# Performance work log

Hardware: AMD Instinct MI355X
Metric: run time of the kernel (lower is better)

## Reference

```python
import jax, jax.numpy as jnp
import numpy as np

B, S, D = 2, 2048, 1024
E, H = 1024, 16
HD = E // H  # head_dim = 64


def setup_inputs() -> dict:
    key = jax.random.key(0)
    k1, k2, k3 = jax.random.split(key, 3)
    x = jax.random.normal(k1, (B, S, D), dtype=jnp.float32)
    # torch Linear weights: [out_features, in_features], xavier_uniform init, zero bias
    lim_qkv = float(np.sqrt(6.0 / (D + 3 * E)))
    w_qkv = jax.random.uniform(k2, (3 * E, D), minval=-lim_qkv, maxval=lim_qkv, dtype=jnp.float32)
    b_qkv = jnp.zeros((3 * E,), dtype=jnp.float32)
    lim_o = float(np.sqrt(6.0 / (E + D)))
    w_out = jax.random.uniform(k3, (D, E), minval=-lim_o, maxval=lim_o, dtype=jnp.float32)
    b_out = jnp.zeros((D,), dtype=jnp.float32)
    return {"x": x, "w_qkv": w_qkv, "b_qkv": b_qkv, "w_out": w_out, "b_out": b_out}


def reference(x, w_qkv, b_qkv, w_out, b_out):
    b, s, _ = x.shape
    qkv = x @ w_qkv.T + b_qkv                       # [B,S,3E]
    qkv = qkv.reshape(b, s, H, 3 * HD).transpose(0, 2, 1, 3)  # [B,H,S,3*HD]
    q, k, v = jnp.split(qkv, 3, axis=-1)            # each [B,H,S,HD]
    # NOTE: source divides by head_dim, not sqrt(head_dim)
    logits = jnp.einsum('bhqd,bhkd->bhqk', q, k) / HD
    attn = jax.nn.softmax(logits, axis=-1)          # [B,H,S,S]
    vals = jnp.einsum('bhqk,bhkd->bhqd', attn, v)   # [B,H,S,HD]
    vals = vals.transpose(0, 2, 1, 3).reshape(b, s, E)
    out = vals @ w_out.T + b_out                    # [B,S,D]
    return out, attn
```

## Files before the change

kernel.cpp:

```cpp
#include <hip/hip_runtime.h>


typedef unsigned short u16;
typedef __attribute__((ext_vector_type(8))) short bf16x8;
typedef __attribute__((ext_vector_type(4))) float f32x4;
typedef __attribute__((ext_vector_type(4))) unsigned int u32x4;
typedef __attribute__((ext_vector_type(4))) unsigned short u16x4;

__device__ __forceinline__ u16 f2b(float f) {
  unsigned u = __builtin_bit_cast(unsigned, f);
  unsigned r = u + 0x7FFFu + ((u >> 16) & 1u);
  return (u16)(r >> 16);
}

__global__ __launch_bounds__(256) void cast_bf16(const float* __restrict__ in,
                                                 u16* __restrict__ out, int n4) {
  int i = blockIdx.x * 256 + threadIdx.x;
  if (i >= n4) return;
  f32x4 v = ((const f32x4*)in)[i];
  u16x4 o;
  o.x = f2b(v.x); o.y = f2b(v.y); o.z = f2b(v.z); o.w = f2b(v.w);
  ((u16x4*)out)[i] = o;
}

template <int EPI>
__global__ __launch_bounds__(256) void gemm_nt(
    const u16* __restrict__ A, const u16* __restrict__ B,
    const float* __restrict__ bias, float* __restrict__ Cout,
    u16* __restrict__ outq, u16* __restrict__ outk, u16* __restrict__ outvT,
    int M, int N, int K) {
  __shared__ u16 lA[128][40];
  __shared__ u16 lB[128][40];
  const int t = threadIdx.x;
  const int lane = t & 63;
  const int w = t >> 6;
  const int wr = w >> 1, wc = w & 1;
  const int l15 = lane & 15, lg = lane >> 4;
  const int m0 = blockIdx.y * 128;
  const int n0 = blockIdx.x * 128;
  const int ldrow = t >> 1;
  const int ldel = (t & 1) * 16;

  f32x4 acc[4][4] = {};

  for (int k0 = 0; k0 < K; k0 += 32) {
    const u16* ga = A + (size_t)(m0 + ldrow) * K + k0 + ldel;
    const u16* gb = B + (size_t)(n0 + ldrow) * K + k0 + ldel;
    u32x4 va0 = *(const u32x4*)ga;
    u32x4 va1 = *(const u32x4*)(ga + 8);
    u32x4 vb0 = *(const u32x4*)gb;
    u32x4 vb1 = *(const u32x4*)(gb + 8);
    *(u32x4*)&lA[ldrow][ldel]     = va0;
    *(u32x4*)&lA[ldrow][ldel + 8] = va1;
    *(u32x4*)&lB[ldrow][ldel]     = vb0;
    *(u32x4*)&lB[ldrow][ldel + 8] = vb1;
    __syncthreads();
    bf16x8 af[4], bf[4];
#pragma unroll
    for (int i = 0; i < 4; i++)
      af[i] = *(const bf16x8*)&lA[64 * wr + 16 * i + l15][8 * lg];
#pragma unroll
    for (int j = 0; j < 4; j++)
      bf[j] = *(const bf16x8*)&lB[64 * wc + 16 * j + l15][8 * lg];
#pragma unroll
    for (int i = 0; i < 4; i++)
#pragma unroll
      for (int j = 0; j < 4; j++)
        acc[i][j] = __builtin_amdgcn_mfma_f32_16x16x32_bf16(af[i], bf[j], acc[i][j], 0, 0, 0);
    __syncthreads();
  }

  const int r0 = lg * 4;
#pragma unroll
  for (int i = 0; i < 4; i++) {
    const int m = m0 + 64 * wr + 16 * i + r0;
#pragma unroll
    for (int j = 0; j < 4; j++) {
      const int n = n0 + 64 * wc + 16 * j + l15;
      const float bv = bias[n];
      if (EPI == 0) {
#pragma unroll
        for (int r = 0; r < 4; r++)
          Cout[(size_t)(m + r) * N + n] = acc[i][j][r] + bv;
      } else {
        const int h = n / 192;
        const int rem = n - h * 192;
        const int which = rem >> 6;
        const int d = rem & 63;
        const int b = m >> 11;
        const int s = m & 2047;
        const size_t bh = (size_t)b * 16 + h;
        u16 o[4];
#pragma unroll
        for (int r = 0; r < 4; r++) o[r] = f2b(acc[i][j][r] + bv);
        if (which == 0) {
#pragma unroll
          for (int r = 0; r < 4; r++)
            outq[(bh * 2048 + s + r) * 64 + d] = o[r];
        } else if (which == 1) {
#pragma unroll
          for (int r = 0; r < 4; r++)
            outk[(bh * 2048 + s + r) * 64 + d] = o[r];
        } else {
          u16x4 pk; pk.x = o[0]; pk.y = o[1]; pk.z = o[2]; pk.w = o[3];
          *(u16x4*)&outvT[(bh * 64 + d) * 2048 + s] = pk;
        }
      }
    }
  }
}

__global__ __launch_bounds__(256) void attn_fused(
    const u16* __restrict__ q, const u16* __restrict__ kk, const u16* __restrict__ vT,
    float* __restrict__ attn, u16* __restrict__ valsb) {
  constexpr int S = 2048, HD = 64;
  __shared__ u16 lQ[64][72];
  __shared__ u16 lK[128][72];
  __shared__ u16 lV[64][136];
  __shared__ u16 lP[64][136];

  const int t = threadIdx.x;
  const int lane = t & 63;
  const int w = t >> 6;
  const int l15 = lane & 15, lg = lane >> 4;
  const int qb = blockIdx.x;
  const int bh = blockIdx.y;
  const size_t qkbase = (size_t)bh * S * HD;
  const float scale = 1.0f / 64.0f;

  {
#pragma unroll
    for (int p = 0; p < 2; p++) {
      int cc = t + p * 256;
      int row = cc >> 3, ch = cc & 7;
      *(u32x4*)&lQ[row][ch * 8] =
          *(const u32x4*)&q[qkbase + (size_t)(qb * 64 + row) * HD + ch * 8];
    }
  }
  __syncthreads();
  bf16x8 aq[2];
#pragma unroll
  for (int s2 = 0; s2 < 2; s2++)
    aq[s2] = *(const bf16x8*)&lQ[16 * w + l15][32 * s2 + 8 * lg];

  float rs[4] = {0.f, 0.f, 0.f, 0.f};

  for (int kt = 0; kt < 16; ++kt) {
    __syncthreads();
#pragma unroll
    for (int p = 0; p < 4; p++) {
      int cc = t + p * 256;
      int row = cc >> 3, ch = cc & 7;
      *(u32x4*)&lK[row][ch * 8] =
          *(const u32x4*)&kk[qkbase + (size_t)(kt * 128 + row) * HD + ch * 8];
    }
    __syncthreads();
#pragma unroll
    for (int j = 0; j < 8; j++) {
      f32x4 sa = {0.f, 0.f, 0.f, 0.f};
#pragma unroll
      for (int s2 = 0; s2 < 2; s2++) {
        bf16x8 bk = *(const bf16x8*)&lK[16 * j + l15][32 * s2 + 8 * lg];
        sa = __builtin_amdgcn_mfma_f32_16x16x32_bf16(aq[s2], bk, sa, 0, 0, 0);
      }
#pragma unroll
      for (int r = 0; r < 4; r++) rs[r] += __expf(sa[r] * scale);
    }
  }
#pragma unroll
  for (int dlt = 1; dlt < 16; dlt <<= 1)
#pragma unroll
    for (int r = 0; r < 4; r++) rs[r] += __shfl_xor(rs[r], dlt, 64);
  float inv[4];
#pragma unroll
  for (int r = 0; r < 4; r++) inv[r] = 1.0f / rs[r];

  f32x4 vacc[4] = {};
  const size_t vbase = (size_t)bh * HD * S;
  for (int kt = 0; kt < 16; ++kt) {
    __syncthreads();
#pragma unroll
    for (int p = 0; p < 4; p++) {
      int cc = t + p * 256;
      int row = cc >> 3, ch = cc & 7;
      *(u32x4*)&lK[row][ch * 8] =
          *(const u32x4*)&kk[qkbase + (size_t)(kt * 128 + row) * HD + ch * 8];
    }
#pragma unroll
    for (int p = 0; p < 4; p++) {
      int cc = t + p * 256;
      int row = cc >> 4, ch = cc & 15;
      *(u32x4*)&lV[row][ch * 8] =
          *(const u32x4*)&vT[vbase + (size_t)row * S + kt * 128 + ch * 8];
    }
    __syncthreads();
#pragma unroll
    for (int j = 0; j < 8; j++) {
      f32x4 sa = {0.f, 0.f, 0.f, 0.f};
#pragma unroll
      for (int s2 = 0; s2 < 2; s2++) {
        bf16x8 bk = *(const bf16x8*)&lK[16 * j + l15][32 * s2 + 8 * lg];
        sa = __builtin_amdgcn_mfma_f32_16x16x32_bf16(aq[s2], bk, sa, 0, 0, 0);
      }
      const size_t abase =
          ((size_t)bh * S + (qb * 64 + 16 * w + 4 * lg)) * S + kt * 128 + 16 * j + l15;
#pragma unroll
      for (int r = 0; r < 4; r++) {
        float pval = __expf(sa[r] * scale) * inv[r];
        attn[abase + (size_t)r * S] = pval;
        lP[16 * w + 4 * lg + r][16 * j + l15] = f2b(pval);
      }
    }
    __syncthreads();
#pragma unroll
    for (int s2 = 0; s2 < 4; s2++) {
      bf16x8 pa = *(const bf16x8*)&lP[16 * w + l15][32 * s2 + 8 * lg];
#pragma unroll
      for (int jd = 0; jd < 4; jd++) {
        bf16x8 bv = *(const bf16x8*)&lV[16 * jd + l15][32 * s2 + 8 * lg];
        vacc[jd] = __builtin_amdgcn_mfma_f32_16x16x32_bf16(pa, bv, vacc[jd], 0, 0, 0);
      }
    }
  }

  const int b = bh >> 4, h = bh & 15;
#pragma unroll
  for (int jd = 0; jd < 4; jd++) {
    const int d = 16 * jd + l15;
#pragma unroll
    for (int r = 0; r < 4; r++) {
      const int srow = qb * 64 + 16 * w + 4 * lg + r;
      valsb[(size_t)(b * 2048 + srow) * 1024 + h * 64 + d] = f2b(vacc[jd][r]);
    }
  }
}

extern "C" void kernel_launch(void* const* d_in, const int* in_sizes, int n_in,
                              void* d_out, int out_size, void* d_ws, size_t ws_size,
                              hipStream_t stream) {
  constexpr int B = 2, S = 2048, D = 1024, E = 1024, H = 16;
  constexpr int M = B * S;
  const float* x     = (const float*)d_in[0];
  const float* w_qkv = (const float*)d_in[1];
  const float* b_qkv = (const float*)d_in[2];
  const float* w_out = (const float*)d_in[3];
  const float* b_out = (const float*)d_in[4];
  float* out  = (float*)d_out;
  float* attn = out + (size_t)M * D;

  char* ws = (char*)d_ws;
  u16* xb    = (u16*)(ws);
  u16* wqkvb = (u16*)(ws + 8388608);
  u16* woutb = (u16*)(ws + 14680064);
  u16* qb    = (u16*)(ws + 16777216);
  u16* kb    = (u16*)(ws + 25165824);
  u16* vTb   = (u16*)(ws + 33554432);
  u16* valsb = (u16*)(ws + 41943040);

  cast_bf16<<<dim3((M * D / 4 + 255) / 256), 256, 0, stream>>>(x, xb, M * D / 4);
  cast_bf16<<<dim3((3 * E * D / 4 + 255) / 256), 256, 0, stream>>>(w_qkv, wqkvb, 3 * E * D / 4);
  cast_bf16<<<dim3((D * E / 4 + 255) / 256), 256, 0, stream>>>(w_out, woutb, D * E / 4);

  gemm_nt<1><<<dim3(3 * E / 128, M / 128), 256, 0, stream>>>(
      xb, wqkvb, b_qkv, nullptr, qb, kb, vTb, M, 3 * E, D);

  attn_fused<<<dim3(S / 64, B * H), 256, 0, stream>>>(qb, kb, vTb, attn, valsb);

  gemm_nt<0><<<dim3(D / 128, M / 128), 256, 0, stream>>>(
      valsb, woutb, b_out, out, nullptr, nullptr, nullptr, M, D, E);
}
```

Before: 730.0 us.

## Use direct-to-LDS loads in GEMM and drop LDS staging in attention

The QKV/out GEMM now stages A and B tiles with global_load_lds (direct global-to-LDS) into unpadded tiles. The attention kernel drops shared-memory staging of Q, K and V. It reads MFMA operands straight from global memory, swaps the MFMA operand order so each lane holds contiguous attention outputs, and writes vectorized f32x4 attn stores. The 1/64 scale and log2e factor are folded into Q in the GEMM epilogue so softmax uses exp2 directly. The goal is fewer syncthreads and LDS round trips and better store coalescing, at the cost of more redundant global/L2 traffic for K and V across waves and possible LDS bank conflicts in the unpadded GEMM tiles.

```diff
diff --git a/kernel.cpp b/kernel.cpp
--- a/kernel.cpp
+++ b/kernel.cpp
@@ -11,6 +11,12 @@
   unsigned u = __builtin_bit_cast(unsigned, f);
   unsigned r = u + 0x7FFFu + ((u >> 16) & 1u);
   return (u16)(r >> 16);
+}
+
+__device__ __forceinline__ void gload_lds16(const u16* g, u16* l) {
+  __builtin_amdgcn_global_load_lds(
+      (const __attribute__((address_space(1))) unsigned int*)(const void*)g,
+      (__attribute__((address_space(3))) unsigned int*)(void*)l, 16, 0, 0);
 }
 
 __global__ __launch_bounds__(256) void cast_bf16(const float* __restrict__ in,
@@ -29,8 +35,8 @@
     const float* __restrict__ bias, float* __restrict__ Cout,
     u16* __restrict__ outq, u16* __restrict__ outk, u16* __restrict__ outvT,
     int M, int N, int K) {
-  __shared__ u16 lA[128][40];
-  __shared__ u16 lB[128][40];
+  __shared__ u16 lA[128][32];
+  __shared__ u16 lB[128][32];
   const int t = threadIdx.x;
   const int lane = t & 63;
   const int w = t >> 6;
@@ -38,22 +44,18 @@
   const int l15 = lane & 15, lg = lane >> 4;
   const int m0 = blockIdx.y * 128;
   const int n0 = blockIdx.x * 128;
-  const int ldrow = t >> 1;
-  const int ldel = (t & 1) * 16;
+  const int ro = lane >> 2;
+  const int co = (lane & 3) * 8;
 
   f32x4 acc[4][4] = {};
 
   for (int k0 = 0; k0 < K; k0 += 32) {
-    const u16* ga = A + (size_t)(m0 + ldrow) * K + k0 + ldel;
-    const u16* gb = B + (size_t)(n0 + ldrow) * K + k0 + ldel;
-    u32x4 va0 = *(const u32x4*)ga;
-    u32x4 va1 = *(const u32x4*)(ga + 8);
-    u32x4 vb0 = *(const u32x4*)gb;
-    u32x4 vb1 = *(const u32x4*)(gb + 8);
-    *(u32x4*)&lA[ldrow][ldel]     = va0;
-    *(u32x4*)&lA[ldrow][ldel + 8] = va1;
-    *(u32x4*)&lB[ldrow][ldel]     = vb0;
-    *(u32x4*)&lB[ldrow][ldel + 8] = vb1;
+    const u16* ga = A + (size_t)(m0 + 32 * w + ro) * K + k0 + co;
+    const u16* gb = B + (size_t)(n0 + 32 * w + ro) * K + k0 + co;
+    gload_lds16(ga,                      &lA[32 * w][0]);
+    gload_lds16(ga + (size_t)16 * K,     &lA[32 * w + 16][0]);
+    gload_lds16(gb,                      &lB[32 * w][0]);
+    gload_lds16(gb + (size_t)16 * K,     &lB[32 * w + 16][0]);
     __syncthreads();
     bf16x8 af[4], bf[4];
 #pragma unroll
@@ -70,6 +72,7 @@
     __syncthreads();
   }
 
+  const float QSCALE = 1.442695041f / 64.0f;
   const int r0 = lg * 4;
 #pragma unroll
   for (int i = 0; i < 4; i++) {
@@ -90,19 +93,18 @@
         const int b = m >> 11;
         const int s = m & 2047;
         const size_t bh = (size_t)b * 16 + h;
-        u16 o[4];
-#pragma unroll
-        for (int r = 0; r < 4; r++) o[r] = f2b(acc[i][j][r] + bv);
         if (which == 0) {
 #pragma unroll
           for (int r = 0; r < 4; r++)
-            outq[(bh * 2048 + s + r) * 64 + d] = o[r];
+            outq[(bh * 2048 + s + r) * 64 + d] = f2b((acc[i][j][r] + bv) * QSCALE);
         } else if (which == 1) {
 #pragma unroll
           for (int r = 0; r < 4; r++)
-            outk[(bh * 2048 + s + r) * 64 + d] = o[r];
+            outk[(bh * 2048 + s + r) * 64 + d] = f2b(acc[i][j][r] + bv);
         } else {
-          u16x4 pk; pk.x = o[0]; pk.y = o[1]; pk.z = o[2]; pk.w = o[3];
+          u16x4 pk;
+          pk.x = f2b(acc[i][j][0] + bv); pk.y = f2b(acc[i][j][1] + bv);
+          pk.z = f2b(acc[i][j][2] + bv); pk.w = f2b(acc[i][j][3] + bv);
           *(u16x4*)&outvT[(bh * 64 + d) * 2048 + s] = pk;
         }
       }
@@ -114,9 +116,6 @@
     const u16* __restrict__ q, const u16* __restrict__ kk, const u16* __restrict__ vT,
     float* __restrict__ attn, u16* __restrict__ valsb) {
   constexpr int S = 2048, HD = 64;
-  __shared__ u16 lQ[64][72];
-  __shared__ u16 lK[128][72];
-  __shared__ u16 lV[64][136];
   __shared__ u16 lP[64][136];
 
   const int t = threadIdx.x;
@@ -126,98 +125,55 @@
   const int qb = blockIdx.x;
   const int bh = blockIdx.y;
   const size_t qkbase = (size_t)bh * S * HD;
-  const float scale = 1.0f / 64.0f;
-
-  {
-#pragma unroll
-    for (int p = 0; p < 2; p++) {
-      int cc = t + p * 256;
-      int row = cc >> 3, ch = cc & 7;
-      *(u32x4*)&lQ[row][ch * 8] =
-          *(const u32x4*)&q[qkbase + (size_t)(qb * 64 + row) * HD + ch * 8];
-    }
-  }
-  __syncthreads();
-  bf16x8 aq[2];
-#pragma unroll
-  for (int s2 = 0; s2 < 2; s2++)
-    aq[s2] = *(const bf16x8*)&lQ[16 * w + l15][32 * s2 + 8 * lg];
-
-  float rs[4] = {0.f, 0.f, 0.f, 0.f};
-
+  const size_t vbase = (size_t)bh * HD * S;
+  const int qrow = qb * 64 + 16 * w + l15;
+
+  bf16x8 aq0 = *(const bf16x8*)&q[qkbase + (size_t)qrow * HD + 8 * lg];
+  bf16x8 aq1 = *(const bf16x8*)&q[qkbase + (size_t)qrow * HD + 32 + 8 * lg];
+
+  float rs = 0.f;
   for (int kt = 0; kt < 16; ++kt) {
-    __syncthreads();
-#pragma unroll
-    for (int p = 0; p < 4; p++) {
-      int cc = t + p * 256;
-      int row = cc >> 3, ch = cc & 7;
-      *(u32x4*)&lK[row][ch * 8] =
-          *(const u32x4*)&kk[qkbase + (size_t)(kt * 128 + row) * HD + ch * 8];
-    }
-    __syncthreads();
+    const u16* kp = kk + qkbase + (size_t)kt * 128 * HD;
 #pragma unroll
     for (int j = 0; j < 8; j++) {
+      bf16x8 bk0 = *(const bf16x8*)&kp[(size_t)(16 * j + l15) * HD + 8 * lg];
+      bf16x8 bk1 = *(const bf16x8*)&kp[(size_t)(16 * j + l15) * HD + 32 + 8 * lg];
       f32x4 sa = {0.f, 0.f, 0.f, 0.f};
-#pragma unroll
-      for (int s2 = 0; s2 < 2; s2++) {
-        bf16x8 bk = *(const bf16x8*)&lK[16 * j + l15][32 * s2 + 8 * lg];
-        sa = __builtin_amdgcn_mfma_f32_16x16x32_bf16(aq[s2], bk, sa, 0, 0, 0);
-      }
-#pragma unroll
-      for (int r = 0; r < 4; r++) rs[r] += __expf(sa[r] * scale);
-    }
-  }
-#pragma unroll
-  for (int dlt = 1; dlt < 16; dlt <<= 1)
-#pragma unroll
-    for (int r = 0; r < 4; r++) rs[r] += __shfl_xor(rs[r], dlt, 64);
-  float inv[4];
-#pragma unroll
-  for (int r = 0; r < 4; r++) inv[r] = 1.0f / rs[r];
+      sa = __builtin_amdgcn_mfma_f32_16x16x32_bf16(bk0, aq0, sa, 0, 0, 0);
+      sa = __builtin_amdgcn_mfma_f32_16x16x32_bf16(bk1, aq1, sa, 0, 0, 0);
+#pragma unroll
+      for (int r = 0; r < 4; r++) rs += __builtin_exp2f(sa[r]);
+    }
+  }
+  rs += __shfl_xor(rs, 16, 64);
+  rs += __shfl_xor(rs, 32, 64);
+  const float inv = 1.0f / rs;
 
   f32x4 vacc[4] = {};
-  const size_t vbase = (size_t)bh * HD * S;
   for (int kt = 0; kt < 16; ++kt) {
-    __syncthreads();
-#pragma unroll
-    for (int p = 0; p < 4; p++) {
-      int cc = t + p * 256;
-      int row = cc >> 3, ch = cc & 7;
-      *(u32x4*)&lK[row][ch * 8] =
-          *(const u32x4*)&kk[qkbase + (size_t)(kt * 128 + row) * HD + ch * 8];
-    }
-#pragma unroll
-    for (int p = 0; p < 4; p++) {
-      int cc = t + p * 256;
-      int row = cc >> 4, ch = cc & 15;
-      *(u32x4*)&lV[row][ch * 8] =
-          *(const u32x4*)&vT[vbase + (size_t)row * S + kt * 128 + ch * 8];
-    }
-    __syncthreads();
+    const u16* kp = kk + qkbase + (size_t)kt * 128 * HD;
 #pragma unroll
     for (int j = 0; j < 8; j++) {
+      bf16x8 bk0 = *(const bf16x8*)&kp[(size_t)(16 * j + l15) * HD + 8 * lg];
+      bf16x8 bk1 = *(const bf16x8*)&kp[(size_t)(16 * j + l15) * HD + 32 + 8 * lg];
       f32x4 sa = {0.f, 0.f, 0.f, 0.f};
-#pragma unroll
-      for (int s2 = 0; s2 < 2; s2++) {
-        bf16x8 bk = *(const bf16x8*)&lK[16 * j + l15][32 * s2 + 8 * lg];
-        sa = __builtin_amdgcn_mfma_f32_16x16x32_bf16(aq[s2], bk, sa, 0, 0, 0);
-      }
-      const size_t abase =
-          ((size_t)bh * S + (qb * 64 + 16 * w + 4 * lg)) * S + kt * 128 + 16 * j + l15;
-#pragma unroll
-      for (int r = 0; r < 4; r++) {
-        float pval = __expf(sa[r] * scale) * inv[r];
-        attn[abase + (size_t)r * S] = pval;
-        lP[16 * w + 4 * lg + r][16 * j + l15] = f2b(pval);
-      }
-    }
-    __syncthreads();
+      sa = __builtin_amdgcn_mfma_f32_16x16x32_bf16(bk0, aq0, sa, 0, 0, 0);
+      sa = __builtin_amdgcn_mfma_f32_16x16x32_bf16(bk1, aq1, sa, 0, 0, 0);
+      f32x4 pv;
+#pragma unroll
+      for (int r = 0; r < 4; r++) pv[r] = __builtin_exp2f(sa[r]) * inv;
+      *(f32x4*)&attn[((size_t)bh * S + qrow) * S + kt * 128 + 16 * j + 4 * lg] = pv;
+      u16x4 pb;
+      pb.x = f2b(pv[0]); pb.y = f2b(pv[1]); pb.z = f2b(pv[2]); pb.w = f2b(pv[3]);
+      *(u16x4*)&lP[16 * w + l15][16 * j + 4 * lg] = pb;
+    }
 #pragma unroll
     for (int s2 = 0; s2 < 4; s2++) {
       bf16x8 pa = *(const bf16x8*)&lP[16 * w + l15][32 * s2 + 8 * lg];
 #pragma unroll
       for (int jd = 0; jd < 4; jd++) {
-        bf16x8 bv = *(const bf16x8*)&lV[16 * jd + l15][32 * s2 + 8 * lg];
+        bf16x8 bv = *(const bf16x8*)&vT[vbase + (size_t)(16 * jd + l15) * S +
+                                        kt * 128 + 32 * s2 + 8 * lg];
         vacc[jd] = __builtin_amdgcn_mfma_f32_16x16x32_bf16(pa, bv, vacc[jd], 0, 0, 0);
       }
     }
```

After: 1.018 ms. 1.39x slower.
